# Optimization experiments

Measured on AMD Instinct MI355X. Metric: run time of the kernel, lower is better.

The kernel has to match this reference:

```python
import jax, jax.numpy as jnp
import numpy as np

# Bipartite frontier sizes per layer (targets of layer i): fanouts [15,10,5] over 1024 seeds
N_TGT = (60000, 6000, 1024)


def sage_layer(x_src, n_tgt, src, dst, Wl, Wr, b):
    # PyG SAGEConv, aggr='mean', root_weight=True:
    #   out = lin_l(mean_{j in N(i)} x_j) + lin_r(x_i) + bias
    x_tgt = x_src[:n_tgt]                       # [n_tgt, d]
    msg = x_src[src]                            # gather: [E, d]
    agg = jax.ops.segment_sum(msg, dst, num_segments=n_tgt)
    cnt = jax.ops.segment_sum(jnp.ones((src.shape[0], 1), x_src.dtype), dst, num_segments=n_tgt)
    mean = agg / jnp.maximum(cnt, 1.0)          # zero-degree nodes -> 0
    return mean @ Wl + x_tgt @ Wr + b


def setup_inputs() -> dict:
    key = jax.random.key(0)
    ks = jax.random.split(key, 16)
    N0 = 900000
    E = (900000, 60000, 5120)
    dims = [(100, 256), (256, 256), (256, 47)]
    inp = {"x": jax.random.normal(ks[0], (N0, 100), dtype=jnp.float32)}
    n_src = (N0,) + N_TGT[:2]
    for i in range(3):
        inp[f"src{i}"] = jax.random.randint(ks[1 + 2 * i], (E[i],), 0, n_src[i])
        inp[f"dst{i}"] = jax.random.randint(ks[2 + 2 * i], (E[i],), 0, N_TGT[i])
    for i, (din, dout) in enumerate(dims):
        inp[f"Wl{i}"] = jax.random.normal(ks[7 + 3 * i], (din, dout), dtype=jnp.float32) * 0.05
        inp[f"Wr{i}"] = jax.random.normal(ks[8 + 3 * i], (din, dout), dtype=jnp.float32) * 0.05
        inp[f"b{i}"] = jnp.zeros((dout,), dtype=jnp.float32)
    return inp


def reference(x, src0, dst0, src1, dst1, src2, dst2,
              Wl0, Wr0, b0, Wl1, Wr1, b1, Wl2, Wr2, b2):
    srcs = (src0, src1, src2)
    dsts = (dst0, dst1, dst2)
    Wls = (Wl0, Wl1, Wl2)
    Wrs = (Wr0, Wr1, Wr2)
    bs = (b0, b1, b2)
    for i in range(3):
        x = sage_layer(x, N_TGT[i], srcs[i], dsts[i], Wls[i], Wrs[i], bs[i])
        if i != 2:
            x = jax.nn.relu(x)  # dropout is identity in eval mode
    return jax.nn.log_softmax(x, axis=-1)
```

## Files before the change

kernel.cpp:

```cpp
#include <hip/hip_runtime.h>
#include <hip/hip_bf16.h>


typedef short bf16x8 __attribute__((ext_vector_type(8)));
typedef float f32x4 __attribute__((ext_vector_type(4)));

static __device__ __forceinline__ unsigned short f2bf(float f) {
  unsigned u = __float_as_uint(f);
  unsigned r = u + 0x7FFFu + ((u >> 16) & 1u);
  return (unsigned short)(r >> 16);
}
static __device__ __forceinline__ float bf2f_lo(unsigned u) {
  return __uint_as_float(u << 16);
}
static __device__ __forceinline__ float bf2f_hi(unsigned u) {
  return __uint_as_float(u & 0xFFFF0000u);
}
static __device__ __forceinline__ unsigned packbf(float lo, float hi) {
  return ((unsigned)f2bf(hi) << 16) | (unsigned)f2bf(lo);
}

#define E0C 900000
#define E1C 60000
#define E2C 5120
#define ETC 965120
#define HB  3770

#define ROW0_OFF 0
#define ROW1_OFF 60001
#define ROW2_OFF 66002
#define CNT_OFF  67027
#define RANK_OFF 134051
#define SS0_OFF  1099171
#define SS1_OFF  1999171
#define SS2_OFF  2059171

struct TileGeom { int tin, goff, n, T; };
static __device__ __forceinline__ TileGeom tile_geom(int b) {
  TileGeom g;
  if (b < 118)      { g.tin = b;       g.goff = 0;     g.n = 60000; g.T = 118; }
  else if (b < 130) { g.tin = b - 118; g.goff = 60000; g.n = 6000;  g.T = 12; }
  else              { g.tin = b - 130; g.goff = 66000; g.n = 1024;  g.T = 2; }
  return g;
}

__global__ __launch_bounds__(256) void histrank_k(
    const int* __restrict__ d0, const int* __restrict__ d1, const int* __restrict__ d2,
    int* __restrict__ cnt, int* __restrict__ rank) {
  int t = blockIdx.x * 256 + threadIdx.x;
  if (t < E0C) {
    rank[t] = atomicAdd(&cnt[d0[t]], 1);
  } else if (t < E0C + E1C) {
    rank[t] = atomicAdd(&cnt[60000 + d1[t - E0C]], 1);
  } else if (t < ETC) {
    rank[t] = atomicAdd(&cnt[66000 + d2[t - E0C - E1C]], 1);
  }
}

__global__ __launch_bounds__(256) void scanpack_k(
    const int* __restrict__ cnt,
    int* __restrict__ row0, int* __restrict__ row1, int* __restrict__ row2,
    const float* __restrict__ Wl0, const float* __restrict__ Wr0,
    unsigned short* __restrict__ bm0,
    const float* __restrict__ Wl1, const float* __restrict__ Wr1,
    unsigned short* __restrict__ bm1) {
  const int b = blockIdx.x;
  const int tid = threadIdx.x;
  if (b < 132) {
    __shared__ int sc[256];
    const TileGeom g = tile_geom(b);
    int* row = (b < 118) ? row0 : (b < 130 ? row1 : row2);
    int p = 0;
    const int lim = g.tin * 512;
    for (int i = tid; i < lim; i += 256) p += cnt[g.goff + i];
    sc[tid] = p;
    __syncthreads();
    for (int off = 128; off; off >>= 1) {
      if (tid < off) sc[tid] += sc[tid + off];
      __syncthreads();
    }
    const int pref = sc[0];
    __syncthreads();
    const int i0 = g.tin * 512 + 2 * tid;
    const int e0 = (i0 < g.n) ? cnt[g.goff + i0] : 0;
    const int e1 = (i0 + 1 < g.n) ? cnt[g.goff + i0 + 1] : 0;
    sc[tid] = e0 + e1;
    __syncthreads();
    for (int off = 1; off < 256; off <<= 1) {
      int v = (tid >= off) ? sc[tid - off] : 0;
      __syncthreads();
      sc[tid] += v;
      __syncthreads();
    }
    const int excl = sc[tid] - (e0 + e1);
    const int o0 = pref + excl;
    const int o1 = o0 + e0;
    if (i0 < g.n) row[i0] = o0;
    if (i0 + 1 < g.n) row[i0 + 1] = o1;
    if (g.tin == g.T - 1 && tid == 255) row[g.n] = pref + sc[255];
  } else {
    int j = b - 132;
    int n = tid;
    if (j < 224) {
      int k = j;
      float v = 0.f;
      if (k < 100) v = Wl0[(size_t)k * 256 + n];
      else if (k >= 112 && k < 212) v = Wr0[(size_t)(k - 112) * 256 + n];
      bm0[(((size_t)(k >> 3) * 256) + n) * 8 + (k & 7)] = f2bf(v);
    } else {
      int k = j - 224;
      float v = (k < 256) ? Wl1[(size_t)k * 256 + n] : Wr1[(size_t)(k - 256) * 256 + n];
      bm1[(((size_t)(k >> 3) * 256) + n) * 8 + (k & 7)] = f2bf(v);
    }
  }
}

__global__ __launch_bounds__(256) void fillscatter_k(
    const int* __restrict__ d0, const int* __restrict__ d1, const int* __restrict__ d2,
    const int* __restrict__ s0, const int* __restrict__ s1, const int* __restrict__ s2,
    const int* __restrict__ row0, const int* __restrict__ row1,
    const int* __restrict__ row2, const int* __restrict__ rank,
    int* __restrict__ o0, int* __restrict__ o1, int* __restrict__ o2) {
  int t = blockIdx.x * 256 + threadIdx.x;
  if (t < E0C) {
    o0[row0[d0[t]] + rank[t]] = s0[t];
  } else if (t < E0C + E1C) {
    int e = t - E0C;
    o1[row1[d1[e]] + rank[t]] = s1[e];
  } else if (t < ETC) {
    int e = t - E0C - E1C;
    o2[row2[d2[e]] + rank[t]] = s2[e];
  }
}

__global__ __launch_bounds__(256) void gather_fused_k(
    const float* __restrict__ x, const int* __restrict__ ss,
    const int* __restrict__ rs, unsigned short* __restrict__ am, int n) {
  int idx = blockIdx.x * 256 + threadIdx.x;
  int w = idx >> 6;
  int f = idx & 63;
  if (w >= n) return;
  const int lo = rs[w];
  const int hi = rs[w + 1];
  float acc0 = 0.f, acc1 = 0.f;
  const int k1 = f + 64;
  int e = lo;
  for (; e + 4 <= hi; e += 4) {
    const float* p0 = x + (size_t)ss[e] * 100;
    const float* p1 = x + (size_t)ss[e + 1] * 100;
    const float* p2 = x + (size_t)ss[e + 2] * 100;
    const float* p3 = x + (size_t)ss[e + 3] * 100;
    acc0 += (p0[f] + p1[f]) + (p2[f] + p3[f]);
    if (k1 < 100) acc1 += (p0[k1] + p1[k1]) + (p2[k1] + p3[k1]);
  }
  for (; e < hi; ++e) {
    const float* p0 = x + (size_t)ss[e] * 100;
    acc0 += p0[f];
    if (k1 < 100) acc1 += p0[k1];
  }
  const float inv = 1.f / (float)max(hi - lo, 1);
  unsigned short* arow = am + (size_t)w * 224;
  arow[f] = f2bf(acc0 * inv);
  if (k1 < 112) arow[k1] = (k1 < 100) ? f2bf(acc1 * inv) : (unsigned short)0;
  const float* xrow = x + (size_t)w * 100;
  arow[112 + f] = f2bf(xrow[f]);
  if (k1 < 112) arow[112 + k1] = (k1 < 100) ? f2bf(xrow[k1]) : (unsigned short)0;
}

__global__ __launch_bounds__(256) void gather_mean_b16_k(
    const unsigned* __restrict__ xbu, const int* __restrict__ ss,
    const int* __restrict__ rs, unsigned* __restrict__ meanu, int n) {
  int idx = blockIdx.x * 256 + threadIdx.x;
  int w = idx >> 6;
  int f = idx & 63;
  if (w >= n) return;
  const int lo = rs[w];
  const int hi = rs[w + 1];
  float a0l = 0.f, a0h = 0.f, a1l = 0.f, a1h = 0.f;
  int e = lo;
  for (; e + 2 <= hi; e += 2) {
    const unsigned* p0 = xbu + (size_t)ss[e] * 128;
    const unsigned* p1 = xbu + (size_t)ss[e + 1] * 128;
    unsigned u0a = p0[f], u0b = p0[f + 64];
    unsigned u1a = p1[f], u1b = p1[f + 64];
    a0l += bf2f_lo(u0a) + bf2f_lo(u1a);
    a0h += bf2f_hi(u0a) + bf2f_hi(u1a);
    a1l += bf2f_lo(u0b) + bf2f_lo(u1b);
    a1h += bf2f_hi(u0b) + bf2f_hi(u1b);
  }
  for (; e < hi; ++e) {
    const unsigned* p0 = xbu + (size_t)ss[e] * 128;
    unsigned ua = p0[f], ub = p0[f + 64];
    a0l += bf2f_lo(ua); a0h += bf2f_hi(ua);
    a1l += bf2f_lo(ub); a1h += bf2f_hi(ub);
  }
  const float inv = 1.f / (float)max(hi - lo, 1);
  meanu[(size_t)w * 128 + f] = packbf(a0l * inv, a0h * inv);
  meanu[(size_t)w * 128 + f + 64] = packbf(a1l * inv, a1h * inv);
}

__global__ __launch_bounds__(256) void gemm0_k(
    const unsigned short* __restrict__ A, const unsigned short* __restrict__ Bp,
    const float* __restrict__ bias, unsigned short* __restrict__ h0b, int M) {
  constexpr int LDA = 232;
  constexpr int LDC = 264;
  __shared__ unsigned short Sh[64 * LDC];

  const int row0 = blockIdx.x * 64;
  for (int t = threadIdx.x; t < 64 * 28; t += 256) {
    int r = t / 28;
    int c = t - r * 28;
    *reinterpret_cast<uint4*>(&Sh[r * LDA + c * 8]) =
        *reinterpret_cast<const uint4*>(A + (size_t)(row0 + r) * 224 + c * 8);
  }
  __syncthreads();

  const int wid = threadIdx.x >> 6;
  const int l = threadIdx.x & 63;
  const int l15 = l & 15;
  const int lhi = l >> 4;

  f32x4 acc[4][4];
#pragma unroll
  for (int rt = 0; rt < 4; ++rt)
#pragma unroll
    for (int ct = 0; ct < 4; ++ct) acc[rt][ct] = (f32x4){0.f, 0.f, 0.f, 0.f};

  for (int kc = 0; kc < 7; ++kc) {
    bf16x8 a[4], b[4];
#pragma unroll
    for (int rt = 0; rt < 4; ++rt)
      a[rt] = *reinterpret_cast<const bf16x8*>(
          &Sh[(rt * 16 + l15) * LDA + kc * 32 + lhi * 8]);
#pragma unroll
    for (int ct = 0; ct < 4; ++ct) {
      int n = wid * 64 + ct * 16 + l15;
      b[ct] = *reinterpret_cast<const bf16x8*>(
          Bp + ((size_t)(kc * 4 + lhi) * 256 + n) * 8);
    }
#pragma unroll
    for (int rt = 0; rt < 4; ++rt)
#pragma unroll
      for (int ct = 0; ct < 4; ++ct)
        acc[rt][ct] = __builtin_amdgcn_mfma_f32_16x16x32_bf16(a[rt], b[ct],
                                                              acc[rt][ct], 0, 0, 0);
  }
  __syncthreads();

#pragma unroll
  for (int rt = 0; rt < 4; ++rt) {
#pragma unroll
    for (int ct = 0; ct < 4; ++ct) {
      int col = wid * 64 + ct * 16 + l15;
      float bv = bias[col];
#pragma unroll
      for (int r = 0; r < 4; ++r) {
        int rr = rt * 16 + lhi * 4 + r;
        Sh[rr * LDC + col] = f2bf(fmaxf(acc[rt][ct][r] + bv, 0.f));
      }
    }
  }
  __syncthreads();

  const int mrem = M - row0;
  for (int t = threadIdx.x; t < 64 * 32; t += 256) {
    int r = t >> 5;
    int c = t & 31;
    if (r < mrem) {
      *reinterpret_cast<uint4*>(h0b + (size_t)(row0 + r) * 256 + c * 8) =
          *reinterpret_cast<const uint4*>(&Sh[r * LDC + c * 8]);
    }
  }
}

__global__ __launch_bounds__(256) void gemm1_k(
    const unsigned short* __restrict__ A1, const unsigned short* __restrict__ A2,
    const unsigned short* __restrict__ Bp, const float* __restrict__ bias,
    float* __restrict__ h1, int M) {
  constexpr int LDA = 520;
  __shared__ unsigned short As[32 * LDA];

  const int row0 = blockIdx.x * 32;
  for (int t = threadIdx.x; t < 32 * 64; t += 256) {
    int r = t >> 6;
    int c = t & 63;
    const unsigned short* src = (c < 32)
        ? (A1 + (size_t)(row0 + r) * 256 + c * 8)
        : (A2 + (size_t)(row0 + r) * 256 + (c - 32) * 8);
    *reinterpret_cast<uint4*>(&As[r * LDA + c * 8]) =
        *reinterpret_cast<const uint4*>(src);
  }
  __syncthreads();

  const int wid = threadIdx.x >> 6;
  const int l = threadIdx.x & 63;
  const int l15 = l & 15;
  const int lhi = l >> 4;

  f32x4 acc[2][4];
#pragma unroll
  for (int rt = 0; rt < 2; ++rt)
#pragma unroll
    for (int ct = 0; ct < 4; ++ct) acc[rt][ct] = (f32x4){0.f, 0.f, 0.f, 0.f};

  for (int kc = 0; kc < 16; ++kc) {
    bf16x8 a[2], b[4];
#pragma unroll
    for (int rt = 0; rt < 2; ++rt)
      a[rt] = *reinterpret_cast<const bf16x8*>(
          &As[(rt * 16 + l15) * LDA + kc * 32 + lhi * 8]);
#pragma unroll
    for (int ct = 0; ct < 4; ++ct) {
      int n = wid * 64 + ct * 16 + l15;
      b[ct] = *reinterpret_cast<const bf16x8*>(
          Bp + ((size_t)(kc * 4 + lhi) * 256 + n) * 8);
    }
#pragma unroll
    for (int rt = 0; rt < 2; ++rt)
#pragma unroll
      for (int ct = 0; ct < 4; ++ct)
        acc[rt][ct] = __builtin_amdgcn_mfma_f32_16x16x32_bf16(a[rt], b[ct],
                                                              acc[rt][ct], 0, 0, 0);
  }

#pragma unroll
  for (int rt = 0; rt < 2; ++rt) {
#pragma unroll
    for (int ct = 0; ct < 4; ++ct) {
      int col = wid * 64 + ct * 16 + l15;
      float bv = bias[col];
#pragma unroll
      for (int r = 0; r < 4; ++r) {
        int row = row0 + rt * 16 + lhi * 4 + r;
        if (row < M)
          h1[(size_t)row * 256 + col] = fmaxf(acc[rt][ct][r] + bv, 0.f);
      }
    }
  }
}

__global__ __launch_bounds__(256) void final_fused_k(
    const float* __restrict__ h1, const int* __restrict__ ss,
    const int* __restrict__ rs, const float* __restrict__ Wl,
    const float* __restrict__ Wr, const float* __restrict__ bb,
    float* __restrict__ out) {
  __shared__ float sm[4][256];
  __shared__ float sx[4][256];
  const int w = threadIdx.x >> 6;
  const int f = threadIdx.x & 63;
  const int i = blockIdx.x * 4 + w;

  const int lo = rs[i];
  const int hi = rs[i + 1];
  float a0 = 0.f, a1 = 0.f, a2 = 0.f, a3 = 0.f;
  for (int e = lo; e < hi; ++e) {
    const float* p = h1 + (size_t)ss[e] * 256;
    a0 += p[f]; a1 += p[f + 64]; a2 += p[f + 128]; a3 += p[f + 192];
  }
  const float inv = 1.f / (float)max(hi - lo, 1);
  sm[w][f] = a0 * inv; sm[w][f + 64] = a1 * inv;
  sm[w][f + 128] = a2 * inv; sm[w][f + 192] = a3 * inv;
  const float* q = h1 + (size_t)i * 256;
  sx[w][f] = q[f]; sx[w][f + 64] = q[f + 64];
  sx[w][f + 128] = q[f + 128]; sx[w][f + 192] = q[f + 192];

  float acc = -1e30f;
  if (f < 47) {
    float b = bb[f];
    float a = b;
    for (int k = 0; k < 256; ++k) {
      a += sm[w][k] * Wl[k * 47 + f] + sx[w][k] * Wr[k * 47 + f];
    }
    acc = a;
  }
  float m = acc;
#pragma unroll
  for (int off = 32; off; off >>= 1) m = fmaxf(m, __shfl_xor(m, off));
  float e2 = (f < 47) ? expf(acc - m) : 0.f;
  float s = e2;
#pragma unroll
  for (int off = 32; off; off >>= 1) s += __shfl_xor(s, off);
  if (f < 47) out[(size_t)i * 47 + f] = acc - m - logf(s);
}

extern "C" void kernel_launch(void* const* d_in, const int* in_sizes, int n_in,
                              void* d_out, int out_size, void* d_ws, size_t ws_size,
                              hipStream_t stream) {
  const float* x    = (const float*)d_in[0];
  const int*   src0 = (const int*)d_in[1];
  const int*   dst0 = (const int*)d_in[2];
  const int*   src1 = (const int*)d_in[3];
  const int*   dst1 = (const int*)d_in[4];
  const int*   src2 = (const int*)d_in[5];
  const int*   dst2 = (const int*)d_in[6];
  const float* Wl0  = (const float*)d_in[7];
  const float* Wr0  = (const float*)d_in[8];
  const float* b0   = (const float*)d_in[9];
  const float* Wl1  = (const float*)d_in[10];
  const float* Wr1  = (const float*)d_in[11];
  const float* b1   = (const float*)d_in[12];
  const float* Wl2  = (const float*)d_in[13];
  const float* Wr2  = (const float*)d_in[14];
  const float* b2   = (const float*)d_in[15];
  float* out = (float*)d_out;

  const int N0 = 60000, N1 = 6000, N2 = 1024;

  char* base = (char*)d_ws;
  unsigned short* bm0  = (unsigned short*)(base);
  unsigned short* bm1  = (unsigned short*)(base + 114688);
  unsigned short* am0  = (unsigned short*)(base + 376832);
  unsigned short* h0b  = (unsigned short*)(base + 27271168);
  unsigned*       h0bu = (unsigned*)(base + 27271168);
  unsigned short* mean1= (unsigned short*)(base + 58007552);
  unsigned*       mean1u=(unsigned*)(base + 58007552);
  float* h1            = (float*)(base + 61087744);
  int* iw              = (int*)(base + 67248128);
  int* row0 = iw + ROW0_OFF;
  int* row1 = iw + ROW1_OFF;
  int* row2 = iw + ROW2_OFF;
  int* cnt  = iw + CNT_OFF;
  int* rank = iw + RANK_OFF;
  int* ss0  = iw + SS0_OFF;
  int* ss1  = iw + SS1_OFF;
  int* ss2  = iw + SS2_OFF;

  hipMemsetAsync(cnt, 0, (size_t)67024 * sizeof(int), stream);
  histrank_k<<<HB, 256, 0, stream>>>(dst0, dst1, dst2, cnt, rank);
  scanpack_k<<<132 + 736, 256, 0, stream>>>(cnt, row0, row1, row2,
                                            Wl0, Wr0, bm0, Wl1, Wr1, bm1);
  fillscatter_k<<<HB, 256, 0, stream>>>(dst0, dst1, dst2, src0, src1, src2,
                                        row0, row1, row2, rank, ss0, ss1, ss2);

  gather_fused_k<<<(N0 * 64 + 255) / 256, 256, 0, stream>>>(x, ss0, row0, am0, N0);
  gemm0_k<<<(N0 + 63) / 64, 256, 0, stream>>>(am0, bm0, b0, h0b, N0);

  gather_mean_b16_k<<<(N1 * 64 + 255) / 256, 256, 0, stream>>>(
      h0bu, ss1, row1, mean1u, N1);
  gemm1_k<<<(N1 + 31) / 32, 256, 0, stream>>>(mean1, h0b, bm1, b1, h1, N1);

  final_fused_k<<<N2 / 4, 256, 0, stream>>>(h1, ss2, row2, Wl2, Wr2, b2, out);
}
```

Baseline: 255.9 us.

## Split CSR scan into tile-sum and scan-write passes; widen layer-1 gather

Replaces the single scan kernel, where each tile block re-summed every preceding count (quadratic work in the last tiles), with a two-pass scheme. The first pass writes one partial sum per tile, and a new kernel scans those tile sums before writing the row offsets. The layer-1 mean gather now uses two wavefronts per target row, each covering half of the features, with a 4-way unrolled edge loop for more parallelism and memory-level concurrency. This adds one kernel launch and a small tile-sum buffer in the workspace.

```diff
diff --git a/kernel.cpp b/kernel.cpp
--- a/kernel.cpp
+++ b/kernel.cpp
@@ -34,13 +34,14 @@
 #define SS0_OFF  1099171
 #define SS1_OFF  1999171
 #define SS2_OFF  2059171
-
-struct TileGeom { int tin, goff, n, T; };
+#define TSUM_OFF 2064300
+
+struct TileGeom { int tin, goff, n, tbeg, T; };
 static __device__ __forceinline__ TileGeom tile_geom(int b) {
   TileGeom g;
-  if (b < 118)      { g.tin = b;       g.goff = 0;     g.n = 60000; g.T = 118; }
-  else if (b < 130) { g.tin = b - 118; g.goff = 60000; g.n = 6000;  g.T = 12; }
-  else              { g.tin = b - 130; g.goff = 66000; g.n = 1024;  g.T = 2; }
+  if (b < 118)      { g.tin = b;       g.goff = 0;     g.n = 60000; g.tbeg = 0;   g.T = 118; }
+  else if (b < 130) { g.tin = b - 118; g.goff = 60000; g.n = 6000;  g.tbeg = 118; g.T = 12; }
+  else              { g.tin = b - 130; g.goff = 66000; g.n = 1024;  g.tbeg = 130; g.T = 2; }
   return g;
 }
 
@@ -57,9 +58,8 @@
   }
 }
 
-__global__ __launch_bounds__(256) void scanpack_k(
-    const int* __restrict__ cnt,
-    int* __restrict__ row0, int* __restrict__ row1, int* __restrict__ row2,
+__global__ __launch_bounds__(256) void tilesum_pack_k(
+    const int* __restrict__ cnt, int* __restrict__ tsum,
     const float* __restrict__ Wl0, const float* __restrict__ Wr0,
     unsigned short* __restrict__ bm0,
     const float* __restrict__ Wl1, const float* __restrict__ Wr1,
@@ -67,37 +67,19 @@
   const int b = blockIdx.x;
   const int tid = threadIdx.x;
   if (b < 132) {
-    __shared__ int sc[256];
+    __shared__ int red[256];
     const TileGeom g = tile_geom(b);
-    int* row = (b < 118) ? row0 : (b < 130 ? row1 : row2);
-    int p = 0;
-    const int lim = g.tin * 512;
-    for (int i = tid; i < lim; i += 256) p += cnt[g.goff + i];
-    sc[tid] = p;
+    const int i0 = g.tin * 512 + 2 * tid;
+    int s = 0;
+    if (i0 < g.n) s += cnt[g.goff + i0];
+    if (i0 + 1 < g.n) s += cnt[g.goff + i0 + 1];
+    red[tid] = s;
     __syncthreads();
     for (int off = 128; off; off >>= 1) {
-      if (tid < off) sc[tid] += sc[tid + off];
+      if (tid < off) red[tid] += red[tid + off];
       __syncthreads();
     }
-    const int pref = sc[0];
-    __syncthreads();
-    const int i0 = g.tin * 512 + 2 * tid;
-    const int e0 = (i0 < g.n) ? cnt[g.goff + i0] : 0;
-    const int e1 = (i0 + 1 < g.n) ? cnt[g.goff + i0 + 1] : 0;
-    sc[tid] = e0 + e1;
-    __syncthreads();
-    for (int off = 1; off < 256; off <<= 1) {
-      int v = (tid >= off) ? sc[tid - off] : 0;
-      __syncthreads();
-      sc[tid] += v;
-      __syncthreads();
-    }
-    const int excl = sc[tid] - (e0 + e1);
-    const int o0 = pref + excl;
-    const int o1 = o0 + e0;
-    if (i0 < g.n) row[i0] = o0;
-    if (i0 + 1 < g.n) row[i0 + 1] = o1;
-    if (g.tin == g.T - 1 && tid == 255) row[g.n] = pref + sc[255];
+    if (tid == 0) tsum[b] = red[0];
   } else {
     int j = b - 132;
     int n = tid;
@@ -113,6 +95,45 @@
       bm1[(((size_t)(k >> 3) * 256) + n) * 8 + (k & 7)] = f2bf(v);
     }
   }
+}
+
+__global__ __launch_bounds__(256) void scanwrite_k(
+    const int* __restrict__ cnt, const int* __restrict__ tsum,
+    int* __restrict__ row0, int* __restrict__ row1, int* __restrict__ row2) {
+  __shared__ int sc[256];
+  const int b = blockIdx.x;
+  const TileGeom g = tile_geom(b);
+  const int tid = threadIdx.x;
+  int* row = (b < 118) ? row0 : (b < 130 ? row1 : row2);
+
+  int p = 0;
+  for (int t = g.tbeg + tid; t < b; t += 256) p += tsum[t];
+  sc[tid] = p;
+  __syncthreads();
+  for (int off = 128; off; off >>= 1) {
+    if (tid < off) sc[tid] += sc[tid + off];
+    __syncthreads();
+  }
+  const int pref = sc[0];
+  __syncthreads();
+
+  const int i0 = g.tin * 512 + 2 * tid;
+  const int e0 = (i0 < g.n) ? cnt[g.goff + i0] : 0;
+  const int e1 = (i0 + 1 < g.n) ? cnt[g.goff + i0 + 1] : 0;
+  sc[tid] = e0 + e1;
+  __syncthreads();
+  for (int off = 1; off < 256; off <<= 1) {
+    int v = (tid >= off) ? sc[tid - off] : 0;
+    __syncthreads();
+    sc[tid] += v;
+    __syncthreads();
+  }
+  const int excl = sc[tid] - (e0 + e1);
+  const int o0 = pref + excl;
+  const int o1 = o0 + e0;
+  if (i0 < g.n) row[i0] = o0;
+  if (i0 + 1 < g.n) row[i0 + 1] = o1;
+  if (g.tin == g.T - 1 && tid == 255) row[g.n] = pref + sc[255];
 }
 
 __global__ __launch_bounds__(256) void fillscatter_k(
@@ -171,32 +192,31 @@
     const unsigned* __restrict__ xbu, const int* __restrict__ ss,
     const int* __restrict__ rs, unsigned* __restrict__ meanu, int n) {
   int idx = blockIdx.x * 256 + threadIdx.x;
-  int w = idx >> 6;
+  int wp = idx >> 6;
   int f = idx & 63;
+  int w = wp >> 1;
+  int half = wp & 1;
   if (w >= n) return;
   const int lo = rs[w];
   const int hi = rs[w + 1];
-  float a0l = 0.f, a0h = 0.f, a1l = 0.f, a1h = 0.f;
+  const int off = half * 64 + f;
+  float al = 0.f, ah = 0.f;
   int e = lo;
-  for (; e + 2 <= hi; e += 2) {
-    const unsigned* p0 = xbu + (size_t)ss[e] * 128;
-    const unsigned* p1 = xbu + (size_t)ss[e + 1] * 128;
-    unsigned u0a = p0[f], u0b = p0[f + 64];
-    unsigned u1a = p1[f], u1b = p1[f + 64];
-    a0l += bf2f_lo(u0a) + bf2f_lo(u1a);
-    a0h += bf2f_hi(u0a) + bf2f_hi(u1a);
-    a1l += bf2f_lo(u0b) + bf2f_lo(u1b);
-    a1h += bf2f_hi(u0b) + bf2f_hi(u1b);
+  for (; e + 4 <= hi; e += 4) {
+    unsigned u0 = xbu[(size_t)ss[e] * 128 + off];
+    unsigned u1 = xbu[(size_t)ss[e + 1] * 128 + off];
+    unsigned u2 = xbu[(size_t)ss[e + 2] * 128 + off];
+    unsigned u3 = xbu[(size_t)ss[e + 3] * 128 + off];
+    al += (bf2f_lo(u0) + bf2f_lo(u1)) + (bf2f_lo(u2) + bf2f_lo(u3));
+    ah += (bf2f_hi(u0) + bf2f_hi(u1)) + (bf2f_hi(u2) + bf2f_hi(u3));
   }
   for (; e < hi; ++e) {
-    const unsigned* p0 = xbu + (size_t)ss[e] * 128;
-    unsigned ua = p0[f], ub = p0[f + 64];
-    a0l += bf2f_lo(ua); a0h += bf2f_hi(ua);
-    a1l += bf2f_lo(ub); a1h += bf2f_hi(ub);
+    unsigned u0 = xbu[(size_t)ss[e] * 128 + off];
+    al += bf2f_lo(u0);
+    ah += bf2f_hi(u0);
   }
   const float inv = 1.f / (float)max(hi - lo, 1);
-  meanu[(size_t)w * 128 + f] = packbf(a0l * inv, a0h * inv);
-  meanu[(size_t)w * 128 + f + 64] = packbf(a1l * inv, a1h * inv);
+  meanu[(size_t)w * 128 + off] = packbf(al * inv, ah * inv);
 }
 
 __global__ __launch_bounds__(256) void gemm0_k(
@@ -366,8 +386,7 @@
 
   float acc = -1e30f;
   if (f < 47) {
-    float b = bb[f];
-    float a = b;
+    float a = bb[f];
     for (int k = 0; k < 256; ++k) {
       a += sm[w][k] * Wl[k * 47 + f] + sx[w][k] * Wr[k * 47 + f];
     }
@@ -424,18 +443,20 @@
   int* ss0  = iw + SS0_OFF;
   int* ss1  = iw + SS1_OFF;
   int* ss2  = iw + SS2_OFF;
+  int* tsum = iw + TSUM_OFF;
 
   hipMemsetAsync(cnt, 0, (size_t)67024 * sizeof(int), stream);
   histrank_k<<<HB, 256, 0, stream>>>(dst0, dst1, dst2, cnt, rank);
-  scanpack_k<<<132 + 736, 256, 0, stream>>>(cnt, row0, row1, row2,
-                                            Wl0, Wr0, bm0, Wl1, Wr1, bm1);
+  tilesum_pack_k<<<132 + 736, 256, 0, stream>>>(cnt, tsum, Wl0, Wr0, bm0,
+                                                Wl1, Wr1, bm1);
+  scanwrite_k<<<132, 256, 0, stream>>>(cnt, tsum, row0, row1, row2);
   fillscatter_k<<<HB, 256, 0, stream>>>(dst0, dst1, dst2, src0, src1, src2,
                                         row0, row1, row2, rank, ss0, ss1, ss2);
 
   gather_fused_k<<<(N0 * 64 + 255) / 256, 256, 0, stream>>>(x, ss0, row0, am0, N0);
   gemm0_k<<<(N0 + 63) / 64, 256, 0, stream>>>(am0, bm0, b0, h0b, N0);
 
-  gather_mean_b16_k<<<(N1 * 64 + 255) / 256, 256, 0, stream>>>(
+  gather_mean_b16_k<<<(N1 * 2 * 64 + 255) / 256, 256, 0, stream>>>(
       h0bu, ss1, row1, mean1u, N1);
   gemm1_k<<<(N1 + 31) / 32, 256, 0, stream>>>(mean1, h0b, bm1, b1, h1, N1);
 
```

Result: faster. 230.6 us (median of 2 runs) (-9.9%).
